# Kernel tuning notes

Measured on AMD Instinct MI355X. Metric: run time of the kernel, lower is better.

The kernel has to match this reference:

```python
import jax, jax.numpy as jnp
import numpy as np

DEG = np.pi / 180.0
H_FOV = (-180.0 * DEG, 180.0 * DEG)   # azimuth fov (rad)
V_FOV = (-3.0 * DEG, 25.0 * DEG)      # elevation fov (rad), phi = -asin(z/r)
W = 2048  # int((h_fov[1]-h_fov[0]) / h_res), h_res = 360/2048 deg
H = 64    # int((v_fov[1]-v_fov[0]) / v_res), v_res = 28/64 deg
B = 8
N = 2_000_000


def setup_inputs() -> dict:
    key = jax.random.key(0)
    k1, k2, k3 = jax.random.split(key, 3)
    # realistic lidar-scale coordinates: wide xy spread, shallow z
    xyz = jax.random.normal(k1, (N, 3), jnp.float32) * jnp.array([30.0, 30.0, 3.0], jnp.float32)
    inten = jax.random.uniform(k2, (N, 1), dtype=jnp.float32)
    bs = jax.random.randint(k3, (N, 1), 0, B).astype(jnp.float32)  # batch idx stored as float col 0
    points = jnp.concatenate([bs, xyz, inten], axis=1)  # [N, 5]
    return {"points": points, "batch_size": B}


def reference(points, batch_size):
    # points: [N, 1+4] = (batch_idx, x, y, z, intensity)
    bs_idx = points[:, 0].astype(jnp.int32)
    xyz = points[:, 1:4]
    extra = points[:, 4:]

    # spherical projection: r, theta (azimuth, cw from +x), phi (elevation, cw from xy-plane)
    r = jnp.linalg.norm(xyz, axis=1, keepdims=True)                      # [N,1]
    theta = -jnp.arctan2(xyz[:, 1], xyz[:, 0])[:, None]                  # [N,1]
    phi = -jnp.arcsin(xyz[:, 2:3] / jnp.maximum(r, 1e-5))                # [N,1]

    u_n = (theta - H_FOV[0]) / (H_FOV[1] - H_FOV[0])                     # [N,1] normed col
    v_n = (phi - V_FOV[0]) / (V_FOV[1] - V_FOV[0])                       # [N,1] normed row

    mask = (u_n[:, 0] >= 0) & (u_n[:, 0] < 1) & (v_n[:, 0] >= 0) & (v_n[:, 0] < 1)

    u = (u_n[:, 0] * W).astype(jnp.int32)
    v = (v_n[:, 0] * H).astype(jnp.int32)
    # route masked-out points to an out-of-bounds index; scatter mode='drop' discards them
    u = jnp.where(mask, u, W)
    v = jnp.where(mask, v, H)

    # use_xyz=True: features = [xyz, rThetaPhi, raw_features] -> channels = 7
    features = jnp.concatenate([xyz, r, theta, phi, extra], axis=1)      # [N,7]

    rv = jnp.zeros((batch_size, H, W, features.shape[1]), points.dtype)
    rv = rv.at[bs_idx, v, u].set(features, mode='drop')
    return jnp.transpose(rv, (0, 3, 1, 2))  # [B, 7, H, W]
```

## Files before the change

### kernel.cpp

```cpp
#include <hip/hip_runtime.h>
#include <math.h>

#define W_IMG 2048
#define H_IMG 64
#define B_IMG 8
#define C_IMG 7
#define HW_IMG (H_IMG * W_IMG)
#define NPIX (B_IMG * HW_IMG)

typedef float v4f __attribute__((ext_vector_type(4)));

__device__ __forceinline__ float F(unsigned u) { return __uint_as_float(u); }
#define FMAF(a,b,c) __builtin_fmaf((a),(b),(c))

__device__ __forceinline__ float glibc_atanf(float x) {
    const float atanhi[4] = {F(0x3eed6338u), F(0x3f490fdau), F(0x3f7b985eu), F(0x3fc90fdau)};
    const float atanlo[4] = {F(0x31ac3769u), F(0x33222168u), F(0x33140fb4u), F(0x33a22168u)};
    const float aT0 = F(0x3eaaaaabu), aT1 = F(0xbe4ccccdu), aT2 = F(0x3e124925u),
                aT3 = F(0xbde38e38u), aT4 = F(0x3dba2e6eu), aT5 = F(0xbd9d8795u),
                aT6 = F(0x3d886b35u), aT7 = F(0xbd6ef16bu), aT8 = F(0x3d4bda59u),
                aT9 = F(0xbd15a221u), aT10 = F(0x3c8569d7u);

    unsigned hx = __float_as_uint(x);
    unsigned ix = hx & 0x7fffffffu;
    if (ix >= 0x4c800000u) {
        if (ix > 0x7f800000u) return x + x;
        float v = __fadd_rn(atanhi[3], atanlo[3]);
        return (hx >> 31) ? -v : v;
    }
    int id;
    float xr = x;
    if (ix < 0x3ee00000u) {
        if (ix < 0x31000000u) return x;
        id = -1;
    } else {
        xr = fabsf(x);
        if (ix < 0x3f980000u) {
            if (ix < 0x3f300000u) {
                id = 0;
                xr = __fdiv_rn(__fsub_rn(__fmul_rn(2.0f, xr), 1.0f),
                               __fadd_rn(2.0f, xr));
            } else {
                id = 1;
                xr = __fdiv_rn(__fsub_rn(xr, 1.0f), __fadd_rn(xr, 1.0f));
            }
        } else {
            if (ix < 0x401c0000u) {
                id = 2;
                xr = __fdiv_rn(__fsub_rn(xr, 1.5f),
                               __fadd_rn(1.0f, __fmul_rn(1.5f, xr)));
            } else {
                id = 3;
                xr = __fdiv_rn(-1.0f, xr);
            }
        }
    }
    float z = __fmul_rn(xr, xr);
    float w = __fmul_rn(z, z);
    float s1 = __fmul_rn(z, __fadd_rn(aT0, __fmul_rn(w, __fadd_rn(aT2,
               __fmul_rn(w, __fadd_rn(aT4, __fmul_rn(w, __fadd_rn(aT6,
               __fmul_rn(w, __fadd_rn(aT8, __fmul_rn(w, aT10)))))))))));
    float s2 = __fmul_rn(w, __fadd_rn(aT1, __fmul_rn(w, __fadd_rn(aT3,
               __fmul_rn(w, __fadd_rn(aT5, __fmul_rn(w, __fadd_rn(aT7,
               __fmul_rn(w, aT9)))))))));
    if (id < 0) return __fsub_rn(x, __fmul_rn(x, __fadd_rn(s1, s2)));
    float zz = __fsub_rn(atanhi[id],
               __fsub_rn(__fsub_rn(__fmul_rn(xr, __fadd_rn(s1, s2)), atanlo[id]), xr));
    return (hx >> 31) ? -zz : zz;
}

__device__ __forceinline__ float glibc_atan2f(float y, float x) {
    const float pi_o_2 = F(0x3fc90fdbu);
    const float pi     = F(0x40490fdbu);
    const float pi_lo  = F(0xb3bbbd2eu);
    unsigned hx = __float_as_uint(x), hy = __float_as_uint(y);
    unsigned ix = hx & 0x7fffffffu, iy = hy & 0x7fffffffu;
    if (ix > 0x7f800000u || iy > 0x7f800000u) return x + y;
    if (hx == 0x3f800000u) return glibc_atanf(y);
    unsigned m = ((hy >> 31) & 1u) | ((hx >> 30) & 2u);
    if (iy == 0) {
        switch (m) {
            case 0: case 1: return y;
            case 2: return pi;
            default: return -pi;
        }
    }
    if (ix == 0) return (m & 1u) ? -pi_o_2 : pi_o_2;
    if (ix == 0x7f800000u) {
        if (iy == 0x7f800000u) {
            switch (m) {
                case 0: return F(0x3f490fdbu);
                case 1: return -F(0x3f490fdbu);
                case 2: return __fmul_rn(3.0f, F(0x3f490fdbu));
                default: return -__fmul_rn(3.0f, F(0x3f490fdbu));
            }
        } else {
            switch (m) {
                case 0: return 0.0f;
                case 1: return -0.0f;
                case 2: return pi;
                default: return -pi;
            }
        }
    }
    if (iy == 0x7f800000u) return (m & 1u) ? -pi_o_2 : pi_o_2;

    int k = ((int)iy - (int)ix) >> 23;
    float z;
    if (k > 26) {
        z = __fadd_rn(pi_o_2, __fmul_rn(0.5f, pi_lo));
        m &= 1u;
    } else if (k < -26 && (hx >> 31)) {
        z = 0.0f;
    } else {
        z = glibc_atanf(fabsf(__fdiv_rn(y, x)));
    }
    switch (m) {
        case 0: return z;
        case 1: return __uint_as_float(__float_as_uint(z) ^ 0x80000000u);
        case 2: return __fsub_rn(pi, __fsub_rn(z, pi_lo));
        default: return __fsub_rn(__fsub_rn(z, pi_lo), pi);
    }
}

struct Proj {
    float theta, phi;
    int   pix;
    bool  in_image;
};

#define H0F   ((float)(-3.14159265358979323846))
#define SPANH ((float)( 6.28318530717958647692))
#define V0F   ((float)(-3.0 * 3.14159265358979323846 / 180.0))
#define SPANV ((float)((25.0 * 3.14159265358979323846 / 180.0) - \
                       (-3.0 * 3.14159265358979323846 / 180.0)))
#define RHc   (1.0f / SPANH)
#define RVc   (1.0f / SPANV)

__device__ __forceinline__ Proj project_exact(float x, float y, float zr, float bsf) {
    Proj p;
    p.theta = -glibc_atan2f(y, x);
    float s  = __fsqrt_rn(FMAF(-zr, zr, 1.0f));
    float d  = __fadd_rn(1.0f, s);
    p.phi = -__fmul_rn(2.0f, glibc_atan2f(zr, d));

    float u_n = __fmul_rn(__fsub_rn(p.theta, H0F), RHc);
    float v_n = __fmul_rn(__fsub_rn(p.phi,   V0F), RVc);
    p.in_image = (u_n >= 0.0f) && (u_n < 1.0f) && (v_n >= 0.0f) && (v_n < 1.0f);
    p.pix = -1;
    if (p.in_image) {
        int u = (int)__fmul_rn(u_n, (float)W_IMG);
        int v = (int)__fmul_rn(v_n, (float)H_IMG);
        int b = (int)bsf;
        if (u < W_IMG && v < H_IMG) {
            p.pix = (b * H_IMG + v) * W_IMG + u;
        } else {
            p.in_image = false;
        }
    }
    return p;
}

__device__ __forceinline__ float norm_r(float x, float y, float z) {
    return __fsqrt_rn(FMAF(z, z, FMAF(y, y, __fmul_rn(x, x))));
}

__device__ __forceinline__ float atan01(float t) {
    float q = t * t;
    float p =          -0.0117212f;
    p = FMAF(q, p,      0.05265332f);
    p = FMAF(q, p,     -0.11643287f);
    p = FMAF(q, p,      0.19354346f);
    p = FMAF(q, p,     -0.33262347f);
    p = FMAF(q, p,      0.99997726f);
    return t * p;
}

__device__ __forceinline__ void fast_angles(float x, float y, float zr,
                                            float* theta, float* phi) {
    float ax = fabsf(x), ay = fabsf(y);
    float mx = fmaxf(ax, ay), mn = fminf(ax, ay);
    float t = (mx > 0.0f) ? (mn / mx) : 0.0f;
    float a = atan01(t);
    if (ay > ax) a = 1.57079632679f - a;
    if (x < 0.0f) a = 3.14159265359f - a;
    *theta = (y < 0.0f) ? a : -a;

    float az  = fabsf(zr);
    float arg = az / __fsqrt_rn(FMAF(-zr, zr, 1.0f));
    float pa  = atan01(arg);
    *phi = (zr >= 0.0f) ? -pa : pa;
}

#define MU 0.06f
#define MV 0.025f

__global__ void __launch_bounds__(256)
scatter_winner(const float* __restrict__ pts, int* __restrict__ winner, int n) {
    int t = blockIdx.x * blockDim.x + threadIdx.x;
    if (t >= n) return;
    int i = n - 1 - t;
    const float* q = pts + (size_t)i * 5;
    float bsf = q[0], x = q[1], y = q[2], z = q[3];

    float r  = norm_r(x, y, z);
    float zr = __fdiv_rn(z, fmaxf(r, 1e-5f));
    if (zr > 0.05240f || zr < -0.42270f) return;

    float th_a, ph_a;
    fast_angles(x, y, zr, &th_a, &ph_a);
    float uf = (th_a - H0F) * (RHc * (float)W_IMG);
    float vf = (ph_a - V0F) * (RVc * (float)H_IMG);
    float ulo = floorf(uf - MU), uhi = floorf(uf + MU);
    float vlo = floorf(vf - MV), vhi = floorf(vf + MV);

    int pix;
    if (ulo == uhi && vlo == vhi) {
        int u = (int)ulo, v = (int)vlo;
        if (u < 0 || u >= W_IMG || v < 0 || v >= H_IMG) return;
        pix = ((int)bsf * H_IMG + v) * W_IMG + u;
    } else {
        Proj p = project_exact(x, y, zr, bsf);
        if (!p.in_image) return;
        pix = p.pix;
    }

    if (winner[pix] >= i) return;
    atomicMax(&winner[pix], i);
}

__global__ void __launch_bounds__(256, 4)
write_output(const float* __restrict__ pts, const int* __restrict__ winner,
             float* __restrict__ out) {
    int t  = blockIdx.x * blockDim.x + threadIdx.x;
    int p0 = t * 4;
    if (p0 >= NPIX) return;

    int4 w4 = *(const int4*)(winner + p0);
    int wis[4] = {w4.x, w4.y, w4.z, w4.w};

    float qx[4], qy[4], qz[4], qi[4];
#pragma unroll
    for (int k = 0; k < 4; ++k) {
        if (wis[k] >= 0) {
            const float* q = pts + (size_t)wis[k] * 5;
            qx[k] = q[1]; qy[k] = q[2]; qz[k] = q[3]; qi[k] = q[4];
        }
    }

    float fc[C_IMG][4];
#pragma unroll
    for (int c = 0; c < C_IMG; ++c)
#pragma unroll
        for (int k = 0; k < 4; ++k) fc[c][k] = 0.f;

#pragma unroll
    for (int k = 0; k < 4; ++k) {
        if (wis[k] >= 0) {
            float x = qx[k], y = qy[k], z = qz[k];
            float r  = norm_r(x, y, z);
            float zr = __fdiv_rn(z, fmaxf(r, 1e-5f));
            float th, ph;
            fast_angles(x, y, zr, &th, &ph);
            fc[0][k] = x; fc[1][k] = y; fc[2][k] = z;
            fc[3][k] = r; fc[4][k] = th; fc[5][k] = ph;
            fc[6][k] = qi[k];
        }
    }

    int b  = p0 >> 17;
    int hw = p0 & (HW_IMG - 1);
    size_t base = (size_t)b * C_IMG * HW_IMG + hw;
#pragma unroll
    for (int c = 0; c < C_IMG; ++c) {
        v4f v = {fc[c][0], fc[c][1], fc[c][2], fc[c][3]};
        __builtin_nontemporal_store(v, (v4f*)(out + base + (size_t)c * HW_IMG));
    }
}

extern "C" void kernel_launch(void* const* d_in, const int* in_sizes, int n_in,
                              void* d_out, int out_size, void* d_ws, size_t ws_size,
                              hipStream_t stream) {
    const float* pts = (const float*)d_in[0];
    int n = in_sizes[0] / 5;
    int* winner = (int*)d_ws;
    float* out = (float*)d_out;

    scatter_winner<<<(n + 255) / 256, 256, 0, stream>>>(pts, winner, n);

    int pthreads = NPIX / 4;
    write_output<<<(pthreads + 255) / 256, 256, 0, stream>>>(pts, winner, out);
}
```

Measured before the change: 144.9 us.

## Process four points per thread with vector loads and per-axis exact fallback

The scatter kernel becomes a grid-stride loop where each thread loads four consecutive 5-float points as five 16-byte vector loads, resolves each pixel, batches the winner reads, then issues atomicMax. The fast path now uses hardware rcp/rsq approximations instead of correctly rounded division and square root. The exact glibc fallback is split per axis, so only the ambiguous coordinate is recomputed. This targets scalar strided loads and fallback cost, at the risk of lower occupancy and less latency hiding from the capped grid of 1024 blocks.

Measured after the change: 164.2 us. 1.13x slower.

```diff
diff --git a/kernel.cpp b/kernel.cpp
--- a/kernel.cpp
+++ b/kernel.cpp
@@ -123,12 +123,6 @@
     }
 }
 
-struct Proj {
-    float theta, phi;
-    int   pix;
-    bool  in_image;
-};
-
 #define H0F   ((float)(-3.14159265358979323846))
 #define SPANH ((float)( 6.28318530717958647692))
 #define V0F   ((float)(-3.0 * 3.14159265358979323846 / 180.0))
@@ -136,30 +130,6 @@
                        (-3.0 * 3.14159265358979323846 / 180.0)))
 #define RHc   (1.0f / SPANH)
 #define RVc   (1.0f / SPANV)
-
-__device__ __forceinline__ Proj project_exact(float x, float y, float zr, float bsf) {
-    Proj p;
-    p.theta = -glibc_atan2f(y, x);
-    float s  = __fsqrt_rn(FMAF(-zr, zr, 1.0f));
-    float d  = __fadd_rn(1.0f, s);
-    p.phi = -__fmul_rn(2.0f, glibc_atan2f(zr, d));
-
-    float u_n = __fmul_rn(__fsub_rn(p.theta, H0F), RHc);
-    float v_n = __fmul_rn(__fsub_rn(p.phi,   V0F), RVc);
-    p.in_image = (u_n >= 0.0f) && (u_n < 1.0f) && (v_n >= 0.0f) && (v_n < 1.0f);
-    p.pix = -1;
-    if (p.in_image) {
-        int u = (int)__fmul_rn(u_n, (float)W_IMG);
-        int v = (int)__fmul_rn(v_n, (float)H_IMG);
-        int b = (int)bsf;
-        if (u < W_IMG && v < H_IMG) {
-            p.pix = (b * H_IMG + v) * W_IMG + u;
-        } else {
-            p.in_image = false;
-        }
-    }
-    return p;
-}
 
 __device__ __forceinline__ float norm_r(float x, float y, float z) {
     return __fsqrt_rn(FMAF(z, z, FMAF(y, y, __fmul_rn(x, x))));
@@ -176,6 +146,103 @@
     return t * p;
 }
 
+#define MU 0.06f
+#define MV 0.025f
+
+__device__ __forceinline__ int resolve_pix(float bsf, float x, float y, float z) {
+    float r  = norm_r(x, y, z);
+    float zr = __fdiv_rn(z, fmaxf(r, 1e-5f));
+    if (zr > 0.05240f || zr < -0.42270f) return -1;
+
+    float ax = fabsf(x), ay = fabsf(y);
+    float mx = fmaxf(ax, ay), mn = fminf(ax, ay);
+    float t  = (mx > 0.0f) ? (mn * __builtin_amdgcn_rcpf(mx)) : 0.0f;
+    float a  = atan01(t);
+    if (ay > ax) a = 1.57079632679f - a;
+    if (x < 0.0f) a = 3.14159265359f - a;
+    float th = (y < 0.0f) ? a : -a;
+
+    float az  = fabsf(zr);
+    float arg = az * __builtin_amdgcn_rsqf(FMAF(-zr, zr, 1.0f));
+    float pa  = atan01(arg);
+    float ph  = (zr >= 0.0f) ? -pa : pa;
+
+    float uf = (th - H0F) * (RHc * (float)W_IMG);
+    float vf = (ph - V0F) * (RVc * (float)H_IMG);
+    float ulo = floorf(uf - MU), uhi = floorf(uf + MU);
+    float vlo = floorf(vf - MV), vhi = floorf(vf + MV);
+
+    int u, v;
+    if (ulo == uhi) {
+        u = (int)ulo;
+    } else {
+        float theta = -glibc_atan2f(y, x);
+        float u_n = __fmul_rn(__fsub_rn(theta, H0F), RHc);
+        if (!(u_n >= 0.0f && u_n < 1.0f)) return -1;
+        u = (int)__fmul_rn(u_n, (float)W_IMG);
+    }
+    if (u < 0 || u >= W_IMG) return -1;
+
+    if (vlo == vhi) {
+        v = (int)vlo;
+    } else {
+        float s   = __fsqrt_rn(FMAF(-zr, zr, 1.0f));
+        float d   = __fadd_rn(1.0f, s);
+        float phi = -__fmul_rn(2.0f, glibc_atan2f(zr, d));
+        float v_n = __fmul_rn(__fsub_rn(phi, V0F), RVc);
+        if (!(v_n >= 0.0f && v_n < 1.0f)) return -1;
+        v = (int)__fmul_rn(v_n, (float)H_IMG);
+    }
+    if (v < 0 || v >= H_IMG) return -1;
+
+    return (((int)bsf) * H_IMG + v) * W_IMG + u;
+}
+
+#define SC_BLOCKS 1024
+#define SC_TPB    256
+
+__global__ void __launch_bounds__(SC_TPB, 4)
+scatter_winner(const float* __restrict__ pts, int* __restrict__ winner, int n) {
+    const int T = gridDim.x * blockDim.x;
+    const int t = blockIdx.x * blockDim.x + threadIdx.x;
+
+    int rem = n & 3;
+    if (t < rem) {
+        int i = n - 1 - t;
+        const float* q = pts + (size_t)i * 5;
+        int pix = resolve_pix(q[0], q[1], q[2], q[3]);
+        if (pix >= 0 && winner[pix] < i) atomicMax(&winner[pix], i);
+    }
+
+    const int ngrp = n >> 2;
+    for (int g = ngrp - 1 - t; g >= 0; g -= T) {
+        const v4f* p4 = (const v4f*)(pts + (size_t)g * 20);
+        v4f a0 = p4[0], a1 = p4[1], a2 = p4[2], a3 = p4[3], a4 = p4[4];
+        float f[20];
+        *(v4f*)(f +  0) = a0;
+        *(v4f*)(f +  4) = a1;
+        *(v4f*)(f +  8) = a2;
+        *(v4f*)(f + 12) = a3;
+        *(v4f*)(f + 16) = a4;
+
+        int pix[4], idx[4];
+#pragma unroll
+        for (int k = 0; k < 4; ++k) {
+            idx[k] = 4 * g + k;
+            pix[k] = resolve_pix(f[5*k + 0], f[5*k + 1], f[5*k + 2], f[5*k + 3]);
+        }
+
+        int wv[4] = {0x7fffffff, 0x7fffffff, 0x7fffffff, 0x7fffffff};
+#pragma unroll
+        for (int k = 0; k < 4; ++k)
+            if (pix[k] >= 0) wv[k] = winner[pix[k]];
+
+#pragma unroll
+        for (int k = 0; k < 4; ++k)
+            if (pix[k] >= 0 && wv[k] < idx[k]) atomicMax(&winner[pix[k]], idx[k]);
+    }
+}
+
 __device__ __forceinline__ void fast_angles(float x, float y, float zr,
                                             float* theta, float* phi) {
     float ax = fabsf(x), ay = fabsf(y);
@@ -190,43 +257,6 @@
     float arg = az / __fsqrt_rn(FMAF(-zr, zr, 1.0f));
     float pa  = atan01(arg);
     *phi = (zr >= 0.0f) ? -pa : pa;
-}
-
-#define MU 0.06f
-#define MV 0.025f
-
-__global__ void __launch_bounds__(256)
-scatter_winner(const float* __restrict__ pts, int* __restrict__ winner, int n) {
-    int t = blockIdx.x * blockDim.x + threadIdx.x;
-    if (t >= n) return;
-    int i = n - 1 - t;
-    const float* q = pts + (size_t)i * 5;
-    float bsf = q[0], x = q[1], y = q[2], z = q[3];
-
-    float r  = norm_r(x, y, z);
-    float zr = __fdiv_rn(z, fmaxf(r, 1e-5f));
-    if (zr > 0.05240f || zr < -0.42270f) return;
-
-    float th_a, ph_a;
-    fast_angles(x, y, zr, &th_a, &ph_a);
-    float uf = (th_a - H0F) * (RHc * (float)W_IMG);
-    float vf = (ph_a - V0F) * (RVc * (float)H_IMG);
-    float ulo = floorf(uf - MU), uhi = floorf(uf + MU);
-    float vlo = floorf(vf - MV), vhi = floorf(vf + MV);
-
-    int pix;
-    if (ulo == uhi && vlo == vhi) {
-        int u = (int)ulo, v = (int)vlo;
-        if (u < 0 || u >= W_IMG || v < 0 || v >= H_IMG) return;
-        pix = ((int)bsf * H_IMG + v) * W_IMG + u;
-    } else {
-        Proj p = project_exact(x, y, zr, bsf);
-        if (!p.in_image) return;
-        pix = p.pix;
-    }
-
-    if (winner[pix] >= i) return;
-    atomicMax(&winner[pix], i);
 }
 
 __global__ void __launch_bounds__(256, 4)
@@ -283,10 +313,15 @@
                               hipStream_t stream) {
     const float* pts = (const float*)d_in[0];
     int n = in_sizes[0] / 5;
+    if (n <= 0) return;
     int* winner = (int*)d_ws;
     float* out = (float*)d_out;
 
-    scatter_winner<<<(n + 255) / 256, 256, 0, stream>>>(pts, winner, n);
+    int ngrp = n >> 2;
+    int blocks = (ngrp + SC_TPB - 1) / SC_TPB;
+    if (blocks > SC_BLOCKS) blocks = SC_BLOCKS;
+    if (blocks < 1) blocks = 1;
+    scatter_winner<<<blocks, SC_TPB, 0, stream>>>(pts, winner, n);
 
     int pthreads = NPIX / 4;
     write_output<<<(pthreads + 255) / 256, 256, 0, stream>>>(pts, winner, out);
```
